# Optimization experiments

Hardware: AMD Instinct MI355X
Metric: run time of the kernel (lower is better)

The kernel has to match this reference:

```python
import jax, jax.numpy as jnp
import numpy as np
import math

D_MODEL = 1024
NUM_HEADS = 16
D_FF = 4096
EPS = 1e-5
BATCH = 2
SEQ = 2048


def _trunc_normal(key, shape, std):
    # truncated normal on [-3std, 3std], matching nn.init.trunc_normal_
    return std * jax.random.truncated_normal(key, -3.0, 3.0, shape, dtype=jnp.float32)


def setup_inputs() -> dict:
    key = jax.random.key(0)
    ks = jax.random.split(key, 8)
    x = jax.random.normal(ks[0], (BATCH, SEQ, D_MODEL), dtype=jnp.float32)
    std_dd = math.sqrt(2.0 / (D_MODEL + D_MODEL))
    std_up = math.sqrt(2.0 / (D_MODEL + D_FF))
    # Linear stores W as [out_features, in_features]; forward does x @ W.T
    W_q = _trunc_normal(ks[1], (D_MODEL, D_MODEL), std_dd)
    W_k = _trunc_normal(ks[2], (D_MODEL, D_MODEL), std_dd)
    W_v = _trunc_normal(ks[3], (D_MODEL, D_MODEL), std_dd)
    W_o = _trunc_normal(ks[4], (D_MODEL, D_MODEL), std_dd)
    W1 = _trunc_normal(ks[5], (D_FF, D_MODEL), std_up)
    W2 = _trunc_normal(ks[6], (D_MODEL, D_FF), std_up)
    ln1_w = jnp.ones((D_MODEL,), jnp.float32)
    ln1_b = jnp.zeros((D_MODEL,), jnp.float32)
    ln2_w = jnp.ones((D_MODEL,), jnp.float32)
    ln2_b = jnp.zeros((D_MODEL,), jnp.float32)
    return {"x": x, "W_q": W_q, "W_k": W_k, "W_v": W_v, "W_o": W_o,
            "W1": W1, "W2": W2,
            "ln1_w": ln1_w, "ln1_b": ln1_b, "ln2_w": ln2_w, "ln2_b": ln2_b}


def _layernorm(x, w, b):
    xf = x.astype(jnp.float32)
    mean = xf.mean(axis=-1, keepdims=True)
    var = jnp.mean((xf - mean) ** 2, axis=-1, keepdims=True)
    xn = (xf - mean) / jnp.sqrt(var + EPS)
    return (xn * w.astype(jnp.float32) + b.astype(jnp.float32)).astype(x.dtype)


def _attention(x, W_q, W_k, W_v, W_o):
    B, S, D = x.shape
    H, dk = NUM_HEADS, D // NUM_HEADS
    Q = (x @ W_q.T).reshape(B, S, H, dk).transpose(0, 2, 1, 3)  # [B,H,S,dk]
    K = (x @ W_k.T).reshape(B, S, H, dk).transpose(0, 2, 1, 3)
    V = (x @ W_v.T).reshape(B, S, H, dk).transpose(0, 2, 1, 3)
    scores = jnp.einsum('bhqd,bhkd->bhqk', Q, K) / math.sqrt(dk)
    causal = jnp.tril(jnp.ones((S, S), dtype=bool))
    scores = jnp.where(causal, scores, -jnp.inf)
    attn = jax.nn.softmax(scores, axis=-1)
    out = jnp.einsum('bhqk,bhkd->bhqd', attn, V)  # [B,H,S,dk]
    out = out.transpose(0, 2, 1, 3).reshape(B, S, D)
    return out @ W_o.T


def _ffn(x, W1, W2):
    h = x @ W1.T
    h = h * (h > 0)  # ReLU
    return h @ W2.T


def reference(x, W_q, W_k, W_v, W_o, W1, W2, ln1_w, ln1_b, ln2_w, ln2_b):
    x = x + _attention(_layernorm(x, ln1_w, ln1_b), W_q, W_k, W_v, W_o)
    x = x + _ffn(_layernorm(x, ln2_w, ln2_b), W1, W2)
    return x
```

## Files before the change

kernel.cpp:

```cpp
#include <hip/hip_runtime.h>
#include <stdint.h>

typedef unsigned short u16;
typedef __bf16 bf16x8 __attribute__((ext_vector_type(8)));
typedef float f32x4 __attribute__((ext_vector_type(4)));
typedef unsigned short u16x8 __attribute__((ext_vector_type(8)));
typedef unsigned short u16x4 __attribute__((ext_vector_type(4)));
typedef u16x8 u16x8_a __attribute__((may_alias));
typedef u16x4 u16x4_a __attribute__((may_alias));

#define DEV static __device__ __forceinline__

DEV u16 f2bf(float f) {
  unsigned u = __builtin_bit_cast(unsigned, f);
  u += 0x7fffu + ((u >> 16) & 1u);
  return (u16)(u >> 16);
}
DEV bf16x8 ld8(const u16* p) {
  u16x8 v = *(const u16x8_a*)p;
  return __builtin_bit_cast(bf16x8, v);
}
DEV f32x4 vmax4(f32x4 a, f32x4 b) {
  f32x4 r;
  r[0] = fmaxf(a[0], b[0]); r[1] = fmaxf(a[1], b[1]);
  r[2] = fmaxf(a[2], b[2]); r[3] = fmaxf(a[3], b[3]);
  return r;
}
DEV f32x4 shflx4(f32x4 v, int m) {
  f32x4 r;
  r[0] = __shfl_xor(v[0], m); r[1] = __shfl_xor(v[1], m);
  r[2] = __shfl_xor(v[2], m); r[3] = __shfl_xor(v[3], m);
  return r;
}
DEV void swz_block(int& bx, int& by) {
  const int gx = gridDim.x;
  const int nwg = gx * gridDim.y;
  int lin = by * gx + bx;
  const int q = nwg >> 3, r = nwg & 7, x = lin & 7, p = lin >> 3;
  lin = (x < r ? x * (q + 1) : r * (q + 1) + (x - r) * q) + p;
  bx = lin % gx; by = lin / gx;
}

#define GL_LDS16(gp, lp)                                                        \
  __builtin_amdgcn_global_load_lds(                                             \
      (const __attribute__((address_space(1))) void*)(gp),                      \
      (__attribute__((address_space(3))) void*)(lp), 16, 0, 0)

#define VMW8 asm volatile("s_waitcnt vmcnt(8)" ::: "memory")
#define VMW4 asm volatile("s_waitcnt vmcnt(4)" ::: "memory")
#define VMW2 asm volatile("s_waitcnt vmcnt(2)" ::: "memory")
#define VMW0 asm volatile("s_waitcnt vmcnt(0)" ::: "memory")
#define BAR  __builtin_amdgcn_s_barrier()

__global__ __launch_bounds__(256) void cvt_k(const float* __restrict__ s,
                                             u16* __restrict__ d, int n4) {
  int i = blockIdx.x * 256 + threadIdx.x;
  if (i < n4) {
    float4 v = ((const float4*)s)[i];
    u16x4 o;
    o[0] = f2bf(v.x); o[1] = f2bf(v.y); o[2] = f2bf(v.z); o[3] = f2bf(v.w);
    *(u16x4_a*)(d + (size_t)i * 4) = o;
  }
}

__global__ __launch_bounds__(256) void ln_k(const float* __restrict__ x,
                                            const float* __restrict__ w,
                                            const float* __restrict__ b,
                                            u16* __restrict__ o) {
  const int row = blockIdx.x, t = threadIdx.x;
  const float4 v = ((const float4*)(x + (size_t)row * 1024))[t];
  float s = v.x + v.y + v.z + v.w;
  float q = v.x * v.x + v.y * v.y + v.z * v.z + v.w * v.w;
#pragma unroll
  for (int m = 1; m < 64; m <<= 1) { s += __shfl_xor(s, m); q += __shfl_xor(q, m); }
  __shared__ float ss[4], qq[4];
  if ((t & 63) == 0) { ss[t >> 6] = s; qq[t >> 6] = q; }
  __syncthreads();
  s = ss[0] + ss[1] + ss[2] + ss[3];
  q = qq[0] + qq[1] + qq[2] + qq[3];
  const float mean = s * (1.f / 1024.f);
  const float var = q * (1.f / 1024.f) - mean * mean;
  const float rstd = rsqrtf(var + 1e-5f);
  const float4 wv = ((const float4*)w)[t];
  const float4 bv = ((const float4*)b)[t];
  u16x4 ov;
  ov[0] = f2bf((v.x - mean) * rstd * wv.x + bv.x);
  ov[1] = f2bf((v.y - mean) * rstd * wv.y + bv.y);
  ov[2] = f2bf((v.z - mean) * rstd * wv.z + bv.z);
  ov[3] = f2bf((v.w - mean) * rstd * wv.w + bv.w);
  *(u16x4_a*)(o + (size_t)row * 1024 + t * 4) = ov;
}

__global__ __launch_bounds__(256) void vtr_k(const u16* __restrict__ qkvV,
                                             u16* __restrict__ vt) {
  __shared__ u16 T[64][65];
  const int st = blockIdx.x, bh = blockIdx.y;
  const int b = bh >> 4, h = bh & 15;
  const int t = threadIdx.x;
  const u16* src = qkvV + ((size_t)(b * 2048 + st * 64)) * 3072 + h * 64;
  const int r = t >> 2, c0 = (t & 3) * 16;
  u16x8 a0 = *(const u16x8_a*)(src + (size_t)r * 3072 + c0);
  u16x8 a1 = *(const u16x8_a*)(src + (size_t)r * 3072 + c0 + 8);
#pragma unroll
  for (int e = 0; e < 8; ++e) { T[r][c0 + e] = a0[e]; T[r][c0 + 8 + e] = a1[e]; }
  __syncthreads();
  const int d = t >> 2, s0 = (t & 3) * 16;
  u16x8 o0, o1;
#pragma unroll
  for (int e = 0; e < 8; ++e) { o0[e] = T[s0 + e][d]; o1[e] = T[s0 + 8 + e][d]; }
  u16* dst = vt + ((size_t)bh * 64 + d) * 2048 + (size_t)st * 64 + s0;
  *(u16x8_a*)dst = o0;
  *(u16x8_a*)(dst + 8) = o1;
}

DEV void stage_op(const u16* __restrict__ G, int K, int kk, u16* lds, int set,
                  int isB, int w, int l) {
#pragma unroll
  for (int i = 0; i < 2; ++i) {
    const int c = i * 8 + w;
    int rb;
    if (!isB) { const int lr = c * 8; rb = (lr < 64 ? lr : lr + 64) + set * 64; }
    else      { rb = (c >> 2) * 64 + set * 32 + (c & 3) * 8; }
    const int row = rb + (l >> 3);
    const int c8 = (l & 7) ^ (row & 7);
    GL_LDS16(G + (size_t)row * K + kk + c8 * 8, lds + rb * 64);
  }
}
DEV void rdA(const u16* as, int wr, int mh, int l15, int l4, bf16x8 af[4][2]) {
#pragma unroll
  for (int f = 0; f < 4; ++f) {
    const int row = wr * 128 + mh * 64 + f * 16 + l15;
#pragma unroll
    for (int ks = 0; ks < 2; ++ks) {
      const int c8 = (ks * 4 + l4) ^ (row & 7);
      af[f][ks] = ld8(as + row * 64 + c8 * 8);
    }
  }
}
DEV void rdB(const u16* bs, int wc, int nh, int l15, int l4, bf16x8 bf_[2][2]) {
#pragma unroll
  for (int g = 0; g < 2; ++g) {
    const int row = wc * 64 + nh * 32 + g * 16 + l15;
#pragma unroll
    for (int ks = 0; ks < 2; ++ks) {
      const int c8 = (ks * 4 + l4) ^ (row & 7);
      bf_[g][ks] = ld8(bs + row * 64 + c8 * 8);
    }
  }
}

#define MFMA16(mh, nh)                                                          \
  __builtin_amdgcn_s_setprio(1);                                                \
  _Pragma("unroll")                                                             \
  for (int f = 0; f < 4; ++f) {                                                 \
    _Pragma("unroll")                                                           \
    for (int g = 0; g < 2; ++g) {                                               \
      f32x4& a_ = acc[(mh) * 4 + f][(nh) * 2 + g];                              \
      a_ = __builtin_amdgcn_mfma_f32_16x16x32_bf16(af[f][0], bfr[g][0], a_, 0, 0, 0); \
      a_ = __builtin_amdgcn_mfma_f32_16x16x32_bf16(af[f][1], bfr[g][1], a_, 0, 0, 0); \
    }                                                                           \
  }                                                                             \
  __builtin_amdgcn_s_setprio(0);

template <int EPI>
__global__ __launch_bounds__(512, 2) void gemm8(const u16* __restrict__ A,
                                                const u16* __restrict__ Bw,
                                                u16* __restrict__ Cp,
                                                int M, int N, int K, int qcols) {
  __shared__ __align__(16) u16 As[2][256 * 64];
  __shared__ __align__(16) u16 Bs[2][256 * 64];
  const int t = threadIdx.x, w = t >> 6, l = t & 63;
  const int l15 = l & 15, l4 = l >> 4;
  const int wr = w >> 2, wc = w & 3;
  int bx = blockIdx.x, by = blockIdx.y;
  swz_block(bx, by);
  const int bm0 = by * 256, bn0 = bx * 256;
  const u16* Ab = A + (size_t)bm0 * K;
  const u16* Bb = Bw + (size_t)bn0 * K;

  f32x4 acc[8][4] = {};
  stage_op(Ab, K, 0, As[0], 0, 0, w, l);
  stage_op(Bb, K, 0, Bs[0], 0, 1, w, l);
  stage_op(Bb, K, 0, Bs[0], 1, 1, w, l);
  stage_op(Ab, K, 0, As[0], 1, 0, w, l);
  VMW4;
  BAR;

  const int nk = K >> 6;
  int cur = 0;
  bf16x8 af[4][2], bfr[2][2];
  for (int kt = 0; kt < nk; ++kt) {
    const int kn = (kt + 1) << 6;
    const bool more = (kt + 1 < nk);
    u16* An = As[cur ^ 1];
    u16* Bn = Bs[cur ^ 1];
    rdA(As[cur], wr, 0, l15, l4, af);
    rdB(Bs[cur], wc, 0, l15, l4, bfr);
    if (more) stage_op(Ab, K, kn, An, 0, 0, w, l);
    BAR;
    MFMA16(0, 0)
    if (more) { VMW4; } else { VMW2; }
    BAR;
    rdB(Bs[cur], wc, 1, l15, l4, bfr);
    if (more) stage_op(Bb, K, kn, Bn, 0, 1, w, l);
    BAR;
    MFMA16(0, 1)
    if (more) { VMW4; } else { VMW0; }
    BAR;
    rdA(As[cur], wr, 1, l15, l4, af);
    if (more) stage_op(Bb, K, kn, Bn, 1, 1, w, l);
    BAR;
    MFMA16(1, 1)
    BAR;
    rdB(Bs[cur], wc, 0, l15, l4, bfr);
    if (more) stage_op(Ab, K, kn, An, 1, 0, w, l);
    BAR;
    MFMA16(1, 0)
    if (more) { VMW4; }
    BAR;
    cur ^= 1;
  }

#pragma unroll
  for (int m = 0; m < 8; ++m) {
    const int row0 = bm0 + wr * 128 + m * 16 + l4 * 4;
#pragma unroll
    for (int n = 0; n < 4; ++n) {
      const int col = bn0 + wc * 64 + n * 16 + l15;
      const float qs = (col < qcols) ? 0.125f : 1.f;
#pragma unroll
      for (int r = 0; r < 4; ++r) {
        float v = acc[m][n][r] * qs;
        if constexpr (EPI == 1) v = v > 0.f ? v : 0.f;
        Cp[(size_t)(row0 + r) * N + col] = f2bf(v);
      }
    }
  }
}

__global__ __launch_bounds__(512, 1) void gemm128(const u16* __restrict__ A,
                                                  const u16* __restrict__ Bw,
                                                  float* __restrict__ C,
                                                  const float* __restrict__ res,
                                                  int M, int N, int K) {
  __shared__ __align__(16) u16 As[3][128 * 64];
  __shared__ __align__(16) u16 Bs[3][128 * 64];
  const int t = threadIdx.x, w = t >> 6, l = t & 63;
  const int l15 = l & 15, l4 = l >> 4;
  const int wr = w >> 2, wc = w & 3;
  int bx = blockIdx.x, by = blockIdx.y;
  swz_block(bx, by);
  const int bm0 = by * 128, bn0 = bx * 128;
  const u16* Ab = A + (size_t)bm0 * K;
  const u16* Bb = Bw + (size_t)bn0 * K;

  auto stg = [&](const u16* __restrict__ G, u16* lds, int kk) {
#pragma unroll
    for (int i = 0; i < 2; ++i) {
      const int c = i * 8 + w;
      const int row = c * 8 + (l >> 3);
      const int c8 = (l & 7) ^ (row & 7);
      GL_LDS16(G + (size_t)row * K + kk + c8 * 8, lds + c * 512);
    }
  };

  f32x4 acc[4][2] = {};
  stg(Ab, As[0], 0);  stg(Bb, Bs[0], 0);
  stg(Ab, As[1], 64); stg(Bb, Bs[1], 64);
  const int nk = K >> 6;
  for (int kt = 0; kt < nk; ++kt) {
    const int cur = kt % 3;
    if (kt + 2 < nk) {
      const int nxt = (kt + 2) % 3;
      const int kk = (kt + 2) << 6;
      stg(Ab, As[nxt], kk);
      stg(Bb, Bs[nxt], kk);
    }
    const int rem = nk - 1 - kt;
    if (rem >= 2) { VMW8; } else if (rem == 1) { VMW4; } else { VMW0; }
    BAR;
    bf16x8 af[4][2], bfr[2][2];
#pragma unroll
    for (int f = 0; f < 4; ++f) {
      const int row = wr * 64 + f * 16 + l15;
#pragma unroll
      for (int ks = 0; ks < 2; ++ks)
        af[f][ks] = ld8(&As[cur][row * 64 + (((ks * 4 + l4) ^ (row & 7)) * 8)]);
    }
#pragma unroll
    for (int g = 0; g < 2; ++g) {
      const int row = wc * 32 + g * 16 + l15;
#pragma unroll
      for (int ks = 0; ks < 2; ++ks)
        bfr[g][ks] = ld8(&Bs[cur][row * 64 + (((ks * 4 + l4) ^ (row & 7)) * 8)]);
    }
    __builtin_amdgcn_s_setprio(1);
#pragma unroll
    for (int f = 0; f < 4; ++f)
#pragma unroll
      for (int g = 0; g < 2; ++g) {
        acc[f][g] = __builtin_amdgcn_mfma_f32_16x16x32_bf16(af[f][0], bfr[g][0], acc[f][g], 0, 0, 0);
        acc[f][g] = __builtin_amdgcn_mfma_f32_16x16x32_bf16(af[f][1], bfr[g][1], acc[f][g], 0, 0, 0);
      }
    __builtin_amdgcn_s_setprio(0);
    BAR;
  }

#pragma unroll
  for (int f = 0; f < 4; ++f) {
    const int row0 = bm0 + wr * 64 + f * 16 + l4 * 4;
#pragma unroll
    for (int g = 0; g < 2; ++g) {
      const int col = bn0 + wc * 32 + g * 16 + l15;
#pragma unroll
      for (int r = 0; r < 4; ++r) {
        const size_t idx = (size_t)(row0 + r) * N + col;
        C[idx] = res[idx] + acc[f][g][r];
      }
    }
  }
}

__global__ __launch_bounds__(256) void attn_k(const u16* __restrict__ Qm,
                                              const u16* __restrict__ Km,
                                              const u16* __restrict__ vt,
                                              u16* __restrict__ Om) {
  const int S = 2048, D = 1024, ldq = 3072;
  int p = blockIdx.x, bh = blockIdx.y;
  swz_block(p, bh);
  const int bb = bh >> 4, h = bh & 15;
  const int t = threadIdx.x, w = t >> 6, l = t & 63, l15 = l & 15, l4 = l >> 4;
  const float NEGINF = -__builtin_inff();

  __shared__ __align__(16) u16 Ksm[2][64 * 64];
  __shared__ __align__(16) u16 Vsm[2][64 * 64];
  __shared__ __align__(16) u16 Psm[4][16][72];

  const u16* Qb = Qm + (size_t)bb * S * ldq + h * 64;
  const u16* Kb = Km + (size_t)bb * S * ldq + h * 64;
  const u16* Vtb = vt + (size_t)bh * 64 * 2048;

  auto stageKV = [&](int j, int buf) {
    const int k0 = j * 64;
#pragma unroll
    for (int i = 0; i < 2; ++i) {
      const int s = t + i * 256;
      const int row = s >> 3;
      const int colE = ((s & 7) ^ (row & 7)) * 8;
      GL_LDS16(Kb + (size_t)(k0 + row) * ldq + colE, &Ksm[buf][(s >> 6) * 512]);
      GL_LDS16(Vtb + (size_t)row * 2048 + k0 + colE, &Vsm[buf][(s >> 6) * 512]);
    }
  };

  for (int half = 0; half < 2; ++half) {
    const int bx = half ? (31 - p) : p;
    const int q0 = bx * 64;
    __syncthreads();
    stageKV(0, 0);

    bf16x8 qf[2];
    {
      const int qr = q0 + w * 16 + l15;
#pragma unroll
      for (int c = 0; c < 2; ++c) qf[c] = ld8(Qb + (size_t)qr * ldq + c * 32 + l4 * 8);
    }

    f32x4 acc[4] = {};
    f32x4 mrow = {NEGINF, NEGINF, NEGINF, NEGINF};
    f32x4 lrow = {};
    int cur = 0;

    for (int j = 0; j <= bx; ++j) {
      __syncthreads();
      if (j < bx) stageKV(j + 1, cur ^ 1);

      f32x4 sv[4] = {};
      __builtin_amdgcn_s_setprio(1);
#pragma unroll
      for (int c = 0; c < 2; ++c) {
#pragma unroll
        for (int nf = 0; nf < 4; ++nf) {
          const int row = nf * 16 + l15;
          bf16x8 kf = ld8(&Ksm[cur][row * 64 + ((c * 32 + l4 * 8) ^ ((row & 7) * 8))]);
          sv[nf] = __builtin_amdgcn_mfma_f32_16x16x32_bf16(qf[c], kf, sv[nf], 0, 0, 0);
        }
      }
      __builtin_amdgcn_s_setprio(0);

      if (j == bx) {
        const int k0 = j * 64;
#pragma unroll
        for (int nf = 0; nf < 4; ++nf) {
          const int col = k0 + nf * 16 + l15;
#pragma unroll
          for (int r = 0; r < 4; ++r) {
            const int rowq = q0 + w * 16 + l4 * 4 + r;
            if (col > rowq) sv[nf][r] = NEGINF;
          }
        }
      }

      f32x4 mt = vmax4(vmax4(sv[0], sv[1]), vmax4(sv[2], sv[3]));
#pragma unroll
      for (int msk = 1; msk < 16; msk <<= 1) mt = vmax4(mt, shflx4(mt, msk));
      const float grow = fmaxf(fmaxf(mt[0] - mrow[0], mt[1] - mrow[1]),
                               fmaxf(mt[2] - mrow[2], mt[3] - mrow[3]));
      const bool skip = __all(grow <= 8.f);
      f32x4 mnew = skip ? mrow : vmax4(mrow, mt);
      if (!skip) {
        f32x4 sf;
#pragma unroll
        for (int r = 0; r < 4; ++r) sf[r] = __expf(mrow[r] - mnew[r]);
#pragma unroll
        for (int r = 0; r < 4; ++r) lrow[r] *= sf[r];
#pragma unroll
        for (int nf = 0; nf < 4; ++nf) acc[nf] *= sf;
        mrow = mnew;
      }
      f32x4 psum = {};
#pragma unroll
      for (int nf = 0; nf < 4; ++nf) {
#pragma unroll
        for (int r = 0; r < 4; ++r) {
          const float pv = __expf(sv[nf][r] - mnew[r]);
          sv[nf][r] = pv;
          psum[r] += pv;
        }
      }
#pragma unroll
      for (int msk = 1; msk < 16; msk <<= 1) psum += shflx4(psum, msk);
#pragma unroll
      for (int r = 0; r < 4; ++r) lrow[r] += psum[r];

#pragma unroll
      for (int nf = 0; nf < 4; ++nf)
#pragma unroll
        for (int r = 0; r < 4; ++r)
          Psm[w][l4 * 4 + r][nf * 16 + l15] = f2bf(sv[nf][r]);

      __builtin_amdgcn_s_setprio(1);
#pragma unroll
      for (int c = 0; c < 2; ++c) {
        bf16x8 pf = ld8(&Psm[w][l15][c * 32 + l4 * 8]);
#pragma unroll
        for (int nf = 0; nf < 4; ++nf) {
          const int row = nf * 16 + l15;
          bf16x8 vf = ld8(&Vsm[cur][row * 64 + ((c * 32 + l4 * 8) ^ ((row & 7) * 8))]);
          acc[nf] = __builtin_amdgcn_mfma_f32_16x16x32_bf16(pf, vf, acc[nf], 0, 0, 0);
        }
      }
      __builtin_amdgcn_s_setprio(0);
      cur ^= 1;
    }

#pragma unroll
    for (int nf = 0; nf < 4; ++nf) {
      const int col = h * 64 + nf * 16 + l15;
#pragma unroll
      for (int r = 0; r < 4; ++r) {
        const int rowq = q0 + w * 16 + l4 * 4 + r;
        Om[((size_t)bb * S + rowq) * D + col] = f2bf(acc[nf][r] / lrow[r]);
      }
    }
  }
}

extern "C" void kernel_launch(void* const* d_in, const int* in_sizes, int n_in,
                              void* d_out, int out_size, void* d_ws, size_t ws_size,
                              hipStream_t stream) {
  (void)in_sizes; (void)n_in; (void)out_size; (void)ws_size;
  const float* x    = (const float*)d_in[0];
  const float* W_q  = (const float*)d_in[1];
  const float* W_k  = (const float*)d_in[2];
  const float* W_v  = (const float*)d_in[3];
  const float* W_o  = (const float*)d_in[4];
  const float* W1   = (const float*)d_in[5];
  const float* W2   = (const float*)d_in[6];
  const float* ln1w = (const float*)d_in[7];
  const float* ln1b = (const float*)d_in[8];
  const float* ln2w = (const float*)d_in[9];
  const float* ln2b = (const float*)d_in[10];

  const size_t MB = 1ull << 20;
  char* W = (char*)d_ws;
  u16* wqkv  = (u16*)(W + 0);
  u16* wo    = (u16*)(W + 6 * MB);
  u16* w1b   = (u16*)(W + 8 * MB);
  u16* w2b   = (u16*)(W + 16 * MB);
  u16* xn1   = (u16*)(W + 24 * MB);
  u16* qkv   = (u16*)(W + 32 * MB);
  u16* attnb = (u16*)(W + 56 * MB);
  u16* vt    = (u16*)(W + 64 * MB);
  u16* xn2   = (u16*)(W + 64 * MB);
  u16* hbuf  = (u16*)(W + 24 * MB);
  float* x2  = (float*)d_out;

  auto cvt = [&](const float* s, u16* d, int n) {
    int n4 = n >> 2;
    cvt_k<<<dim3((n4 + 255) / 256), dim3(256), 0, stream>>>(s, d, n4);
  };
  cvt(W_q, wqkv, 1 << 20);
  cvt(W_k, wqkv + (1 << 20), 1 << 20);
  cvt(W_v, wqkv + (2 << 20), 1 << 20);
  cvt(W_o, wo, 1 << 20);
  cvt(W1, w1b, 4 << 20);
  cvt(W2, w2b, 4 << 20);

  ln_k<<<dim3(4096), dim3(256), 0, stream>>>(x, ln1w, ln1b, xn1);
  gemm8<0><<<dim3(12, 16), dim3(512), 0, stream>>>(xn1, wqkv, qkv, 4096, 3072, 1024, 1024);
  vtr_k<<<dim3(32, 32), dim3(256), 0, stream>>>(qkv + 2048, vt);
  attn_k<<<dim3(16, 32), dim3(256), 0, stream>>>(qkv, qkv + 1024, vt, attnb);
  gemm128<<<dim3(8, 32), dim3(512), 0, stream>>>(attnb, wo, x2, x, 4096, 1024, 1024);
  ln_k<<<dim3(4096), dim3(256), 0, stream>>>(x2, ln2w, ln2b, xn2);
  gemm8<1><<<dim3(16, 16), dim3(512), 0, stream>>>(xn2, w1b, hbuf, 4096, 4096, 1024, 0);
  gemm128<<<dim3(8, 32), dim3(512), 0, stream>>>(hbuf, w2b, x2, x2, 4096, 1024, 4096);
}
```

Before: 266.0 us.

## Transpose attention MFMA operands so each lane owns one query row

Swaps the MFMA operand order in the attention kernel so scores and output are computed transposed. Each lane then holds a single query row, which turns the per-row max and sum reductions into scalar work with two cross-lane shuffles instead of sixteen. P is packed to bf16 with v_cvt_pk_bf16_f32 and written to a swizzled u32 LDS buffer, and the output is stored as 4-wide vectors. This cuts shuffle, softmax and store instruction counts, at the cost of a more complex swizzled P layout in LDS.

```diff
diff --git a/kernel.cpp b/kernel.cpp
--- a/kernel.cpp
+++ b/kernel.cpp
@@ -2,6 +2,7 @@
 #include <stdint.h>
 
 typedef unsigned short u16;
+typedef unsigned int u32;
 typedef __bf16 bf16x8 __attribute__((ext_vector_type(8)));
 typedef float f32x4 __attribute__((ext_vector_type(4)));
 typedef unsigned short u16x8 __attribute__((ext_vector_type(8)));
@@ -24,12 +25,6 @@
   f32x4 r;
   r[0] = fmaxf(a[0], b[0]); r[1] = fmaxf(a[1], b[1]);
   r[2] = fmaxf(a[2], b[2]); r[3] = fmaxf(a[3], b[3]);
-  return r;
-}
-DEV f32x4 shflx4(f32x4 v, int m) {
-  f32x4 r;
-  r[0] = __shfl_xor(v[0], m); r[1] = __shfl_xor(v[1], m);
-  r[2] = __shfl_xor(v[2], m); r[3] = __shfl_xor(v[3], m);
   return r;
 }
 DEV void swz_block(int& bx, int& by) {
@@ -334,7 +329,7 @@
 
   __shared__ __align__(16) u16 Ksm[2][64 * 64];
   __shared__ __align__(16) u16 Vsm[2][64 * 64];
-  __shared__ __align__(16) u16 Psm[4][16][72];
+  __shared__ __align__(16) u32 Psm[4][16 * 32];
 
   const u16* Qb = Qm + (size_t)bb * S * ldq + h * 64;
   const u16* Kb = Km + (size_t)bb * S * ldq + h * 64;
@@ -352,6 +347,10 @@
     }
   };
 
+  u32* Pw = &Psm[w][0];
+  const u16* Pu = (const u16*)Pw;
+  const int h7 = l15 & 7;
+
   for (int half = 0; half < 2; ++half) {
     const int bx = half ? (31 - p) : p;
     const int q0 = bx * 64;
@@ -359,15 +358,12 @@
     stageKV(0, 0);
 
     bf16x8 qf[2];
-    {
-      const int qr = q0 + w * 16 + l15;
-#pragma unroll
-      for (int c = 0; c < 2; ++c) qf[c] = ld8(Qb + (size_t)qr * ldq + c * 32 + l4 * 8);
-    }
-
-    f32x4 acc[4] = {};
-    f32x4 mrow = {NEGINF, NEGINF, NEGINF, NEGINF};
-    f32x4 lrow = {};
+    const int qq = q0 + w * 16 + l15;
+#pragma unroll
+    for (int c = 0; c < 2; ++c) qf[c] = ld8(Qb + (size_t)qq * ldq + c * 32 + l4 * 8);
+
+    f32x4 accT[4] = {};
+    float mrow = NEGINF, lrow = 0.f;
     int cur = 0;
 
     for (int j = 0; j <= bx; ++j) {
@@ -382,7 +378,7 @@
         for (int nf = 0; nf < 4; ++nf) {
           const int row = nf * 16 + l15;
           bf16x8 kf = ld8(&Ksm[cur][row * 64 + ((c * 32 + l4 * 8) ^ ((row & 7) * 8))]);
-          sv[nf] = __builtin_amdgcn_mfma_f32_16x16x32_bf16(qf[c], kf, sv[nf], 0, 0, 0);
+          sv[nf] = __builtin_amdgcn_mfma_f32_16x16x32_bf16(kf, qf[c], sv[nf], 0, 0, 0);
         }
       }
       __builtin_amdgcn_s_setprio(0);
@@ -391,76 +387,70 @@
         const int k0 = j * 64;
 #pragma unroll
         for (int nf = 0; nf < 4; ++nf) {
-          const int col = k0 + nf * 16 + l15;
-#pragma unroll
-          for (int r = 0; r < 4; ++r) {
-            const int rowq = q0 + w * 16 + l4 * 4 + r;
-            if (col > rowq) sv[nf][r] = NEGINF;
-          }
+          const int kb = k0 + nf * 16 + l4 * 4;
+#pragma unroll
+          for (int r = 0; r < 4; ++r)
+            if (kb + r > qq) sv[nf][r] = NEGINF;
         }
       }
 
-      f32x4 mt = vmax4(vmax4(sv[0], sv[1]), vmax4(sv[2], sv[3]));
-#pragma unroll
-      for (int msk = 1; msk < 16; msk <<= 1) mt = vmax4(mt, shflx4(mt, msk));
-      const float grow = fmaxf(fmaxf(mt[0] - mrow[0], mt[1] - mrow[1]),
-                               fmaxf(mt[2] - mrow[2], mt[3] - mrow[3]));
-      const bool skip = __all(grow <= 8.f);
-      f32x4 mnew = skip ? mrow : vmax4(mrow, mt);
+      f32x4 m4 = vmax4(vmax4(sv[0], sv[1]), vmax4(sv[2], sv[3]));
+      float mt = fmaxf(fmaxf(m4[0], m4[1]), fmaxf(m4[2], m4[3]));
+      mt = fmaxf(mt, __shfl_xor(mt, 16));
+      mt = fmaxf(mt, __shfl_xor(mt, 32));
+      const bool skip = __all(mt - mrow <= 8.f);
+      const float mnew = skip ? mrow : fmaxf(mrow, mt);
       if (!skip) {
-        f32x4 sf;
-#pragma unroll
-        for (int r = 0; r < 4; ++r) sf[r] = __expf(mrow[r] - mnew[r]);
-#pragma unroll
-        for (int r = 0; r < 4; ++r) lrow[r] *= sf[r];
-#pragma unroll
-        for (int nf = 0; nf < 4; ++nf) acc[nf] *= sf;
+        const float sf = __expf(mrow - mnew);
+        lrow *= sf;
+#pragma unroll
+        for (int nf = 0; nf < 4; ++nf) accT[nf] *= sf;
         mrow = mnew;
       }
-      f32x4 psum = {};
+#pragma unroll
+      for (int nf = 0; nf < 4; ++nf)
+#pragma unroll
+        for (int r = 0; r < 4; ++r) sv[nf][r] = __expf(sv[nf][r] - mnew);
+      f32x4 s4 = (sv[0] + sv[1]) + (sv[2] + sv[3]);
+      float ps = (s4[0] + s4[1]) + (s4[2] + s4[3]);
+      ps += __shfl_xor(ps, 16);
+      ps += __shfl_xor(ps, 32);
+      lrow += ps;
+
 #pragma unroll
       for (int nf = 0; nf < 4; ++nf) {
-#pragma unroll
-        for (int r = 0; r < 4; ++r) {
-          const float pv = __expf(sv[nf][r] - mnew[r]);
-          sv[nf][r] = pv;
-          psum[r] += pv;
-        }
-      }
-#pragma unroll
-      for (int msk = 1; msk < 16; msk <<= 1) psum += shflx4(psum, msk);
-#pragma unroll
-      for (int r = 0; r < 4; ++r) lrow[r] += psum[r];
-
-#pragma unroll
-      for (int nf = 0; nf < 4; ++nf)
-#pragma unroll
-        for (int r = 0; r < 4; ++r)
-          Psm[w][l4 * 4 + r][nf * 16 + l15] = f2bf(sv[nf][r]);
+        u32 lo, hi;
+        asm("v_cvt_pk_bf16_f32 %0, %1, %2" : "=v"(lo) : "v"(sv[nf][0]), "v"(sv[nf][1]));
+        asm("v_cvt_pk_bf16_f32 %0, %1, %2" : "=v"(hi) : "v"(sv[nf][2]), "v"(sv[nf][3]));
+        const int kw4 = (nf * 2 + (l4 >> 1)) ^ h7;
+        const int base = l15 * 32 + kw4 * 4 + (l4 & 1) * 2;
+        Pw[base] = lo;
+        Pw[base + 1] = hi;
+      }
 
       __builtin_amdgcn_s_setprio(1);
 #pragma unroll
       for (int c = 0; c < 2; ++c) {
-        bf16x8 pf = ld8(&Psm[w][l15][c * 32 + l4 * 8]);
+        bf16x8 pf = ld8(Pu + l15 * 64 + ((c * 4 + l4) ^ h7) * 8);
 #pragma unroll
         for (int nf = 0; nf < 4; ++nf) {
           const int row = nf * 16 + l15;
           bf16x8 vf = ld8(&Vsm[cur][row * 64 + ((c * 32 + l4 * 8) ^ ((row & 7) * 8))]);
-          acc[nf] = __builtin_amdgcn_mfma_f32_16x16x32_bf16(pf, vf, acc[nf], 0, 0, 0);
+          accT[nf] = __builtin_amdgcn_mfma_f32_16x16x32_bf16(vf, pf, accT[nf], 0, 0, 0);
         }
       }
       __builtin_amdgcn_s_setprio(0);
       cur ^= 1;
     }
 
+    const float inv = 1.f / lrow;
+    u16* orow = Om + ((size_t)bb * S + qq) * D + h * 64;
 #pragma unroll
     for (int nf = 0; nf < 4; ++nf) {
-      const int col = h * 64 + nf * 16 + l15;
-#pragma unroll
-      for (int r = 0; r < 4; ++r) {
-        const int rowq = q0 + w * 16 + l4 * 4 + r;
-        Om[((size_t)bb * S + rowq) * D + col] = f2bf(acc[nf][r] / lrow[r]);
-      }
+      u16x4 ov;
+#pragma unroll
+      for (int r = 0; r < 4; ++r) ov[r] = f2bf(accT[nf][r] * inv);
+      *(u16x4_a*)(orow + nf * 16 + l4 * 4) = ov;
     }
   }
 }
```

After: 246.0 us. -7.5%, faster.
